# Performance work log

Measured on AMD Instinct MI355X. Metric: run time of the kernel, lower is better.

Reference implementation:

```python
import jax, jax.numpy as jnp
import numpy as np

B, T, C, H = 4, 2048, 1024, 16
D = C // H  # head_dim = 64


def setup_inputs() -> dict:
    key = jax.random.key(0)
    ks = jax.random.split(key, 5)
    s = 0.02
    return {
        "x": jax.random.normal(ks[0], (B, T, C), dtype=jnp.float32),
        "w_qkv": jax.random.normal(ks[1], (C, 3 * C), dtype=jnp.float32) * s,
        "b_qkv": jnp.zeros((3 * C,), dtype=jnp.float32),
        "w_proj": jax.random.normal(ks[2], (C, C), dtype=jnp.float32) * s,
        "b_proj": jnp.zeros((C,), dtype=jnp.float32),
    }


def reference(x, w_qkv, b_qkv, w_proj, b_proj):
    Bx, Tx, Cx = x.shape
    qkv = x @ w_qkv + b_qkv                      # [B,T,3C]
    q, k, v = jnp.split(qkv, 3, axis=-1)
    # [B,T,C] -> [B,H,T,D]
    q = q.reshape(Bx, Tx, H, D).transpose(0, 2, 1, 3)
    k = k.reshape(Bx, Tx, H, D).transpose(0, 2, 1, 3)
    v = v.reshape(Bx, Tx, H, D).transpose(0, 2, 1, 3)
    scale = 1.0 / np.sqrt(D).astype(np.float32)
    attn = jnp.einsum('bhqd,bhkd->bhqk', q, k) * scale   # [B,H,T,T]
    causal = jnp.tril(jnp.ones((Tx, Tx), dtype=bool))
    attn = jnp.where(causal[None, None], attn, -jnp.inf)
    attn = jax.nn.softmax(attn, axis=-1)
    out = jnp.einsum('bhqk,bhkd->bhqd', attn, v)          # [B,H,T,D]
    out = out.transpose(0, 2, 1, 3).reshape(Bx, Tx, Cx)   # [B,T,C]
    return out @ w_proj + b_proj
```

## Files before the change

kernel.cpp:

```cpp
#include <hip/hip_runtime.h>
#include <hip/hip_bf16.h>
#include <math.h>

using bf16 = __hip_bfloat16;
typedef __bf16 bf16x8 __attribute__((ext_vector_type(8)));
typedef float  f32x4  __attribute__((ext_vector_type(4)));
typedef unsigned short ushort8 __attribute__((ext_vector_type(8)));
typedef unsigned uint4v __attribute__((ext_vector_type(4)));

#define DEV __device__ __forceinline__

DEV void gld_lds16(const void* g, void* l) {
    __builtin_amdgcn_global_load_lds((const __attribute__((address_space(1))) void*)g,
                                     (__attribute__((address_space(3))) void*)l,
                                     16, 0, 0);
}

__global__ __launch_bounds__(256) void prep(const float* __restrict__ x,
                                            bf16* __restrict__ xb,
                                            const float* __restrict__ w_qkv,
                                            bf16* __restrict__ wqkvT,
                                            const float* __restrict__ w_proj,
                                            bf16* __restrict__ wprojT) {
    __shared__ float tile[32][33];
    int blk = blockIdx.x;
    int tid = threadIdx.x;
    if (blk < 8192) {
        int i = blk * 256 + tid;
        float4 f = ((const float4*)x)[i];
        __align__(8) bf16 o[4] = {__float2bfloat16(f.x), __float2bfloat16(f.y),
                                  __float2bfloat16(f.z), __float2bfloat16(f.w)};
        ((uint64_t*)xb)[i] = *(const uint64_t*)o;
        return;
    }
    const float* in;
    bf16* out;
    int R, Cn, bx, by;
    if (blk < 11264) {
        int bid = blk - 8192;
        in = w_qkv; out = wqkvT; R = 1024; Cn = 3072;
        bx = (bid % 96) * 32; by = (bid / 96) * 32;
    } else {
        int bid = blk - 11264;
        in = w_proj; out = wprojT; R = 1024; Cn = 1024;
        bx = (bid % 32) * 32; by = (bid / 32) * 32;
    }
    int tx = tid & 31, ty = tid >> 5;
    for (int i = ty; i < 32; i += 8)
        tile[i][tx] = in[(size_t)(by + i) * Cn + bx + tx];
    __syncthreads();
    for (int i = ty; i < 32; i += 8)
        out[(size_t)(bx + i) * R + by + tx] = __float2bfloat16(tile[tx][i]);
}

__global__ __launch_bounds__(256) void gemm_qkv(const bf16* __restrict__ A,
                                                const bf16* __restrict__ Bt,
                                                const float* __restrict__ bias,
                                                bf16* __restrict__ qb,
                                                bf16* __restrict__ kb,
                                                bf16* __restrict__ vTb) {
    constexpr int K = 1024, T = 2048;
    constexpr float CS = 0.18033688f;
    __shared__ __align__(16) bf16 SM[4][128 * 32];
    bf16* Et = &SM[0][0];
    int tid = threadIdx.x;
    int lane = tid & 63, w = tid >> 6;
    int wm = w >> 1, wn = w & 1;
    int l15 = lane & 15, quad = lane >> 4;
    int m0 = blockIdx.x * 128, n0 = blockIdx.y * 128;
    int l3 = l15 & 3;

    int e0 = tid * 8, e1 = (256 + tid) * 8;
    int r0 = e0 >> 5, c0 = ((((e0 >> 3) & 3) ^ (r0 & 3)) << 3);
    int r1 = e1 >> 5, c1 = ((((e1 >> 3) & 3) ^ (r1 & 3)) << 3);

    f32x4 acc[4][4] = {};

    auto STAGE = [&](int buf, int kc) {
        gld_lds16(A  + (size_t)(m0 + r0) * K + kc + c0, &SM[buf][e0]);
        gld_lds16(A  + (size_t)(m0 + r1) * K + kc + c1, &SM[buf][e1]);
        gld_lds16(Bt + (size_t)(n0 + r0) * K + kc + c0, &SM[2 + buf][e0]);
        gld_lds16(Bt + (size_t)(n0 + r1) * K + kc + c1, &SM[2 + buf][e1]);
    };
    auto COMP = [&](int buf) {
        bf16x8 af[4], bfr[4];
        for (int i = 0; i < 4; ++i)
            af[i] = *(const bf16x8*)&SM[buf][(wm * 64 + i * 16 + l15) * 32 + ((quad ^ l3) << 3)];
        for (int j = 0; j < 4; ++j)
            bfr[j] = *(const bf16x8*)&SM[2 + buf][(wn * 64 + j * 16 + l15) * 32 + ((quad ^ l3) << 3)];
        for (int i = 0; i < 4; ++i)
            for (int j = 0; j < 4; ++j)
                acc[i][j] = __builtin_amdgcn_mfma_f32_16x16x32_bf16(af[i], bfr[j], acc[i][j], 0, 0, 0);
    };

    STAGE(0, 0);
    for (int t = 0; t < K / 64; ++t) {
        int k0 = t * 64;
        __syncthreads();
        STAGE(1, k0 + 32);
        COMP(0);
        __syncthreads();
        if (t + 1 < K / 64) STAGE(0, k0 + 64);
        COMP(1);
    }

    int mode = (blockIdx.y < 8) ? 0 : (blockIdx.y < 16 ? 1 : 2);
    float bv[4];
    for (int j = 0; j < 4; ++j)
        bv[j] = bias[n0 + wn * 64 + j * 16 + l15];
    float scl = (mode == 0) ? CS : 1.0f;

    for (int i = 0; i < 4; ++i) {
        __syncthreads();
        for (int j = 0; j < 4; ++j)
            for (int v = 0; v < 4; ++v)
                Et[(wm * 16 + quad * 4 + v) * 136 + wn * 64 + j * 16 + l15] =
                    __float2bfloat16((acc[i][j][v] + bv[j]) * scl);
        __syncthreads();
        if (mode < 2) {
            int r = tid >> 3, cc = (tid & 7) * 16;
            int m = m0 + i * 16 + (r < 16 ? r : r + 48);
            int b = m >> 11, t = m & 2047;
            int n = (n0 & 1023) + cc;
            int h = n >> 6, d = n & 63;
            bf16* dst = (mode == 0 ? qb : kb) + (((size_t)(b * 16 + h)) * T + t) * 64 + d;
            ushort8 u0 = *(const ushort8*)&Et[r * 136 + cc];
            ushort8 u1 = *(const ushort8*)&Et[r * 136 + cc + 8];
            *(ushort8*)dst = u0;
            *(ushort8*)(dst + 8) = u1;
        } else {
            int run = tid >> 7, d = tid & 127;
            int t0 = m0 + i * 16 + run * 64;
            int b = t0 >> 11, tt = t0 & 2047;
            int n = (n0 & 1023) + d;
            int h = n >> 6, dd = n & 63;
            __align__(16) bf16 tmp[16];
            for (int jj = 0; jj < 16; ++jj)
                tmp[jj] = Et[(run * 16 + jj) * 136 + d];
            bf16* dst = vTb + (((size_t)(b * 16 + h)) * 64 + dd) * T + tt;
            *(ushort8*)dst = *(const ushort8*)tmp;
            *(ushort8*)(dst + 8) = *(const ushort8*)(tmp + 8);
        }
    }
}

__global__ __launch_bounds__(256, 4) void flash_attn(const bf16* __restrict__ qb,
                                                     const bf16* __restrict__ kbuf,
                                                     const bf16* __restrict__ vT,
                                                     bf16* __restrict__ ob) {
    constexpr int T = 2048;
    __shared__ __align__(16) bf16 Kl[2][64 * 64];
    __shared__ __align__(16) bf16 Vl[64 * 64];
    int tid = threadIdx.x;
    int lane = tid & 63, w = tid >> 6;
    int l15 = lane & 15, quad = lane >> 4;

    int g = blockIdx.x;
    int quarter = g >> 8;
    int j = (g >> 6) & 3;
    int bh = g & 63;
    int xq;
    switch (quarter) {
        case 0:  xq = 15 - j; break;
        case 1:  xq = 8 + j;  break;
        case 2:  xq = 4 + j;  break;
        default: xq = 3 - j;  break;
    }
    int q0 = xq << 7;
    const bf16* qbase = qb   + (size_t)bh * T * 64;
    const bf16* kbase = kbuf + (size_t)bh * T * 64;
    const bf16* vbase = vT   + (size_t)bh * 64 * T;

    int qg[2];
    bf16x8 qa[2][2];
#pragma unroll
    for (int s = 0; s < 2; ++s) {
        qg[s] = q0 + w * 32 + s * 16 + l15;
#pragma unroll
        for (int c = 0; c < 2; ++c)
            qa[s][c] = *(const bf16x8*)(qbase + (size_t)qg[s] * 64 + c * 32 + quad * 8);
    }

    bf16x8 ones;
#pragma unroll
    for (int i = 0; i < 8; ++i) ones[i] = (__bf16)1.0f;

    f32x4 O[2][4] = {};
    f32x4 O1[2] = {};
    int h7 = l15 & 7;

    int off0 = tid * 8, off1 = (256 + tid) * 8;
    int r0 = off0 >> 6, cb0 = (off0 >> 3) & 7;
    int r1 = off1 >> 6, cb1 = (off1 >> 3) & 7;
    int kc0 = (cb0 ^ (r0 & 7)) << 3, kc1 = (cb1 ^ (r1 & 7)) << 3;

    int nit = 2 * xq + 2;

    bf16x8 vr0 = *(const bf16x8*)(vbase + (size_t)r0 * T + kc0);
    bf16x8 vr1 = *(const bf16x8*)(vbase + (size_t)r1 * T + kc1);
    gld_lds16(kbase + (size_t)r0 * 64 + kc0, &Kl[0][off0]);
    gld_lds16(kbase + (size_t)r1 * 64 + kc1, &Kl[0][off1]);
    *(bf16x8*)&Vl[off0] = vr0;
    *(bf16x8*)&Vl[off1] = vr1;

    for (int t = 0; t < nit; ++t) {
        int cur = t & 1;
        __syncthreads();
        bool pre = (t + 1 < nit);
        if (pre) {
            int kb2 = (t + 1) << 6, nxt = cur ^ 1;
            vr0 = *(const bf16x8*)(vbase + (size_t)r0 * T + kb2 + kc0);
            vr1 = *(const bf16x8*)(vbase + (size_t)r1 * T + kb2 + kc1);
            gld_lds16(kbase + (size_t)(kb2 + r0) * 64 + kc0, &Kl[nxt][off0]);
            gld_lds16(kbase + (size_t)(kb2 + r1) * 64 + kc1, &Kl[nxt][off1]);
        }
        int kb = t << 6;
        bool maskt = (t >= nit - 2);

        unsigned Dq[2][4][2];
#pragma unroll
        for (int jn = 0; jn < 4; ++jn) {
            int row = jn * 16 + l15;
            bf16x8 a0 = *(const bf16x8*)&Kl[cur][row * 64 + ((quad ^ h7) << 3)];
            bf16x8 a1 = *(const bf16x8*)&Kl[cur][row * 64 + (((4 + quad) ^ h7) << 3)];
            f32x4 sa[2] = {};
            __builtin_amdgcn_s_setprio(1);
            sa[0] = __builtin_amdgcn_mfma_f32_16x16x32_bf16(a0, qa[0][0], sa[0], 0, 0, 0);
            sa[0] = __builtin_amdgcn_mfma_f32_16x16x32_bf16(a1, qa[0][1], sa[0], 0, 0, 0);
            sa[1] = __builtin_amdgcn_mfma_f32_16x16x32_bf16(a0, qa[1][0], sa[1], 0, 0, 0);
            sa[1] = __builtin_amdgcn_mfma_f32_16x16x32_bf16(a1, qa[1][1], sa[1], 0, 0, 0);
            __builtin_amdgcn_s_setprio(0);
#pragma unroll
            for (int s = 0; s < 2; ++s) {
                float p[4];
#pragma unroll
                for (int v = 0; v < 4; ++v) {
                    float e = __builtin_amdgcn_exp2f(sa[s][v]);
                    if (maskt) {
                        int key = kb + jn * 16 + quad * 4 + v;
                        e = (key <= qg[s]) ? e : 0.f;
                    }
                    p[v] = e;
                }
                unsigned lo, hi;
                asm("v_cvt_pk_bf16_f32 %0, %1, %2" : "=v"(lo) : "v"(p[0]), "v"(p[1]));
                asm("v_cvt_pk_bf16_f32 %0, %1, %2" : "=v"(hi) : "v"(p[2]), "v"(p[3]));
                Dq[s][jn][0] = lo;
                Dq[s][jn][1] = hi;
            }
        }

        bf16x8 pf[2][2];
#pragma unroll
        for (int s = 0; s < 2; ++s)
#pragma unroll
            for (int c = 0; c < 2; ++c) {
                uint4v wv;
#pragma unroll
                for (int h = 0; h < 2; ++h) {
                    unsigned X = Dq[s][2 * c][h];
                    unsigned Y = Dq[s][2 * c + 1][h];
                    asm("v_permlane32_swap_b32 %0, %1" : "+v"(X), "+v"(Y));
                    asm("v_permlane16_swap_b32 %0, %1" : "+v"(X), "+v"(Y));
                    wv[h]     = X;
                    wv[2 + h] = Y;
                }
                pf[s][c] = __builtin_bit_cast(bf16x8, wv);
            }

        __builtin_amdgcn_s_setprio(1);
#pragma unroll
        for (int s = 0; s < 2; ++s) {
            O1[s] = __builtin_amdgcn_mfma_f32_16x16x32_bf16(pf[s][0], ones, O1[s], 0, 0, 0);
            O1[s] = __builtin_amdgcn_mfma_f32_16x16x32_bf16(pf[s][1], ones, O1[s], 0, 0, 0);
        }
        __builtin_amdgcn_s_setprio(0);

#pragma unroll
        for (int jd = 0; jd < 4; ++jd) {
            int vrow = jd * 16 + l15;
            bf16x8 v0 = *(const bf16x8*)&Vl[vrow * 64 + ((quad ^ h7) << 3)];
            bf16x8 v1 = *(const bf16x8*)&Vl[vrow * 64 + (((4 + quad) ^ h7) << 3)];
            __builtin_amdgcn_s_setprio(1);
            O[0][jd] = __builtin_amdgcn_mfma_f32_16x16x32_bf16(pf[0][0], v0, O[0][jd], 0, 0, 0);
            O[0][jd] = __builtin_amdgcn_mfma_f32_16x16x32_bf16(pf[0][1], v1, O[0][jd], 0, 0, 0);
            O[1][jd] = __builtin_amdgcn_mfma_f32_16x16x32_bf16(pf[1][0], v0, O[1][jd], 0, 0, 0);
            O[1][jd] = __builtin_amdgcn_mfma_f32_16x16x32_bf16(pf[1][1], v1, O[1][jd], 0, 0, 0);
            __builtin_amdgcn_s_setprio(0);
        }

        __builtin_amdgcn_s_barrier();
        if (pre) {
            *(bf16x8*)&Vl[off0] = vr0;
            *(bf16x8*)&Vl[off1] = vr1;
        }
    }

    int b = bh >> 4, h = bh & 15;
#pragma unroll
    for (int s = 0; s < 2; ++s) {
        float linv[4];
#pragma unroll
        for (int v = 0; v < 4; ++v) linv[v] = 1.f / O1[s][v];
#pragma unroll
        for (int jd = 0; jd < 4; ++jd) {
#pragma unroll
            for (int v = 0; v < 4; ++v) {
                int qr = q0 + w * 32 + s * 16 + quad * 4 + v;
                ob[((size_t)(b * T + qr)) * 1024 + h * 64 + jd * 16 + l15] =
                    __float2bfloat16(O[s][jd][v] * linv[v]);
            }
        }
    }
}

__global__ __launch_bounds__(256) void gemm_proj(const bf16* __restrict__ A,
                                                 const bf16* __restrict__ Bt,
                                                 const float* __restrict__ bias,
                                                 float* __restrict__ out) {
    constexpr int K = 1024, N = 1024;
    __shared__ __align__(16) bf16 SM[4][128 * 32];
    int tid = threadIdx.x;
    int lane = tid & 63, w = tid >> 6;
    int wm = w >> 1, wn = w & 1;
    int l15 = lane & 15, quad = lane >> 4;
    int m0 = blockIdx.x * 128, n0 = blockIdx.y * 128;
    int l3 = l15 & 3;

    int e0 = tid * 8, e1 = (256 + tid) * 8;
    int r0 = e0 >> 5, c0 = ((((e0 >> 3) & 3) ^ (r0 & 3)) << 3);
    int r1 = e1 >> 5, c1 = ((((e1 >> 3) & 3) ^ (r1 & 3)) << 3);

    f32x4 acc[4][4] = {};

    auto STAGE = [&](int buf, int kc) {
        gld_lds16(A  + (size_t)(m0 + r0) * K + kc + c0, &SM[buf][e0]);
        gld_lds16(A  + (size_t)(m0 + r1) * K + kc + c1, &SM[buf][e1]);
        gld_lds16(Bt + (size_t)(n0 + r0) * K + kc + c0, &SM[2 + buf][e0]);
        gld_lds16(Bt + (size_t)(n0 + r1) * K + kc + c1, &SM[2 + buf][e1]);
    };
    auto COMP = [&](int buf) {
        bf16x8 af[4], bfr[4];
        for (int i = 0; i < 4; ++i)
            af[i] = *(const bf16x8*)&SM[buf][(wm * 64 + i * 16 + l15) * 32 + ((quad ^ l3) << 3)];
        for (int j = 0; j < 4; ++j)
            bfr[j] = *(const bf16x8*)&SM[2 + buf][(wn * 64 + j * 16 + l15) * 32 + ((quad ^ l3) << 3)];
        for (int i = 0; i < 4; ++i)
            for (int j = 0; j < 4; ++j)
                acc[i][j] = __builtin_amdgcn_mfma_f32_16x16x32_bf16(af[i], bfr[j], acc[i][j], 0, 0, 0);
    };

    STAGE(0, 0);
    for (int t = 0; t < K / 64; ++t) {
        int k0 = t * 64;
        __syncthreads();
        STAGE(1, k0 + 32);
        COMP(0);
        __syncthreads();
        if (t + 1 < K / 64) STAGE(0, k0 + 64);
        COMP(1);
    }

    for (int i = 0; i < 4; ++i) {
        int mbase = m0 + wm * 64 + i * 16 + quad * 4;
        for (int j = 0; j < 4; ++j) {
            int n = n0 + wn * 64 + j * 16 + l15;
            float bv = bias[n];
            for (int v = 0; v < 4; ++v)
                out[(size_t)(mbase + v) * N + n] = acc[i][j][v] + bv;
        }
    }
}

extern "C" void kernel_launch(void* const* d_in, const int* in_sizes, int n_in,
                              void* d_out, int out_size, void* d_ws, size_t ws_size,
                              hipStream_t stream) {
    (void)in_sizes; (void)n_in; (void)out_size; (void)ws_size;
    const float* x      = (const float*)d_in[0];
    const float* w_qkv  = (const float*)d_in[1];
    const float* b_qkv  = (const float*)d_in[2];
    const float* w_proj = (const float*)d_in[3];
    const float* b_proj = (const float*)d_in[4];
    float* out = (float*)d_out;

    char* ws = (char*)d_ws;
    bf16* xb     = (bf16*)(ws);
    bf16* wqkvT  = (bf16*)(ws + (16u << 20));
    bf16* wprojT = (bf16*)(ws + (22u << 20));
    bf16* qbuf   = (bf16*)(ws + (24u << 20));
    bf16* kbuf   = (bf16*)(ws + (40u << 20));
    bf16* vTb    = (bf16*)(ws + (72u << 20));
    bf16* ob     = (bf16*)(ws + (56u << 20));

    prep<<<12288, 256, 0, stream>>>(x, xb, w_qkv, wqkvT, w_proj, wprojT);
    gemm_qkv<<<dim3(64, 24), 256, 0, stream>>>(xb, wqkvT, b_qkv, qbuf, kbuf, vTb);
    flash_attn<<<1024, 256, 0, stream>>>(qbuf, kbuf, vTb, ob);
    gemm_proj<<<dim3(64, 8), 256, 0, stream>>>(ob, wprojT, b_proj, out);
}
```

Before: 237.5 us.

## Retile QKV GEMM to 128x256 with 512 threads, 64-wide K stages, swizzled grid

The QKV projection GEMM moves from 128x128 tiles with 256 threads and 32-wide K slices to 128x256 tiles with 512 threads (8 waves), 64-wide K slices, an XOR-swizzled LDS layout over 8 column groups, and a remapped block order that groups blocks along the N dimension for L2 reuse. MFMA sections get raised priority via s_setprio. The aim is to cut global/LDS traffic per flop and halve the number of K-loop barriers. In exchange it uses 96KB of LDS per block, which lowers occupancy, and the epilogue is rewritten for the wider tile. The attention and projection kernels are only moved in the file, not changed.

Result: no change. 240.7 us (+1.4%).

```diff
diff --git a/kernel.cpp b/kernel.cpp
--- a/kernel.cpp
+++ b/kernel.cpp
@@ -53,16 +53,292 @@
         out[(size_t)(bx + i) * R + by + tx] = __float2bfloat16(tile[tx][i]);
 }
 
-__global__ __launch_bounds__(256) void gemm_qkv(const bf16* __restrict__ A,
+__global__ __launch_bounds__(512) void gemm_qkv(const bf16* __restrict__ A,
                                                 const bf16* __restrict__ Bt,
                                                 const float* __restrict__ bias,
                                                 bf16* __restrict__ qb,
                                                 bf16* __restrict__ kb,
                                                 bf16* __restrict__ vTb) {
-    constexpr int K = 1024, T = 2048;
+    constexpr int K = 1024;
     constexpr float CS = 0.18033688f;
+    __shared__ __align__(16) bf16 SM[49152];
+    int tid = threadIdx.x;
+    int lane = tid & 63, wid = tid >> 6;
+    int wm = wid >> 2, wn = wid & 3;
+    int l15 = lane & 15, quad = lane >> 4;
+    int h7 = l15 & 7;
+
+    int wg = blockIdx.x;
+    int swz = (wg & 7) * 96 + (wg >> 3);
+    int bx = swz & 63, by = swz >> 6;
+    int m0 = bx * 128, n0 = by * 256;
+
+    int r0s = tid >> 3;
+    int sc0 = (((tid & 7) ^ (r0s & 7)) << 3);
+
+    f32x4 acc[4][4] = {};
+
+#define STAGE(buf, kt) do {                                                        \
+    gld_lds16(A  + (size_t)(m0 + r0s)       * K + (kt) * 64 + sc0,                 \
+              &SM[(buf) * 8192 + tid * 8]);                                        \
+    gld_lds16(A  + (size_t)(m0 + 64 + r0s)  * K + (kt) * 64 + sc0,                 \
+              &SM[(buf) * 8192 + 4096 + tid * 8]);                                 \
+    gld_lds16(Bt + (size_t)(n0 + r0s)       * K + (kt) * 64 + sc0,                 \
+              &SM[16384 + (buf) * 16384 + tid * 8]);                               \
+    gld_lds16(Bt + (size_t)(n0 + 64 + r0s)  * K + (kt) * 64 + sc0,                 \
+              &SM[16384 + (buf) * 16384 + 4096 + tid * 8]);                        \
+    gld_lds16(Bt + (size_t)(n0 + 128 + r0s) * K + (kt) * 64 + sc0,                 \
+              &SM[16384 + (buf) * 16384 + 8192 + tid * 8]);                        \
+    gld_lds16(Bt + (size_t)(n0 + 192 + r0s) * K + (kt) * 64 + sc0,                 \
+              &SM[16384 + (buf) * 16384 + 12288 + tid * 8]);                       \
+} while (0)
+
+#define COMP(buf) do {                                                             \
+    bf16x8 afr[4][2], bfr[4][2];                                                   \
+    for (int i = 0; i < 4; ++i)                                                    \
+        for (int kc = 0; kc < 2; ++kc)                                             \
+            afr[i][kc] = *(const bf16x8*)&SM[(buf) * 8192 +                        \
+                (wm * 64 + i * 16 + l15) * 64 + (((kc * 4 + quad) ^ h7) << 3)];    \
+    for (int nj = 0; nj < 4; ++nj)                                                 \
+        for (int kc = 0; kc < 2; ++kc)                                             \
+            bfr[nj][kc] = *(const bf16x8*)&SM[16384 + (buf) * 16384 +              \
+                (wn * 64 + nj * 16 + l15) * 64 + (((kc * 4 + quad) ^ h7) << 3)];   \
+    __builtin_amdgcn_s_setprio(1);                                                 \
+    for (int i = 0; i < 4; ++i)                                                    \
+        for (int nj = 0; nj < 4; ++nj)                                             \
+            for (int kc = 0; kc < 2; ++kc)                                         \
+                acc[i][nj] = __builtin_amdgcn_mfma_f32_16x16x32_bf16(              \
+                    afr[i][kc], bfr[nj][kc], acc[i][nj], 0, 0, 0);                 \
+    __builtin_amdgcn_s_setprio(0);                                                 \
+} while (0)
+
+    STAGE(0, 0);
+    for (int t2 = 0; t2 < 8; ++t2) {
+        __syncthreads();
+        STAGE(1, 2 * t2 + 1);
+        COMP(0);
+        __syncthreads();
+        if (t2 < 7) STAGE(0, 2 * t2 + 2);
+        COMP(1);
+    }
+#undef STAGE
+#undef COMP
+
+    int mode = by >> 2;
+    float scl = (mode == 0) ? CS : 1.0f;
+    float bv[4];
+    for (int nj = 0; nj < 4; ++nj)
+        bv[nj] = bias[n0 + wn * 64 + nj * 16 + l15];
+    bf16* Et = &SM[0];
+
+    for (int i = 0; i < 4; ++i) {
+        __syncthreads();
+        for (int nj = 0; nj < 4; ++nj)
+            for (int v = 0; v < 4; ++v)
+                Et[(wm * 16 + quad * 4 + v) * 264 + wn * 64 + nj * 16 + l15] =
+                    __float2bfloat16((acc[i][nj][v] + bv[nj]) * scl);
+        __syncthreads();
+        if (mode < 2) {
+            int r = tid >> 4, ck = tid & 15;
+            int m = m0 + i * 16 + (r < 16 ? r : r + 48);
+            int b = m >> 11, t = m & 2047;
+            int n = (n0 & 1023) + ck * 16;
+            int h = n >> 6, d = n & 63;
+            bf16* dst = (mode == 0 ? qb : kb) + (((size_t)(b * 16 + h)) * 2048 + t) * 64 + d;
+            *(ushort8*)dst       = *(const ushort8*)&Et[r * 264 + ck * 16];
+            *(ushort8*)(dst + 8) = *(const ushort8*)&Et[r * 264 + ck * 16 + 8];
+        } else {
+            int tg = tid >> 8, d = tid & 255;
+            int t0 = m0 + tg * 64 + i * 16;
+            int b = t0 >> 11, tt = t0 & 2047;
+            int n = (n0 & 1023) + d;
+            int h = n >> 6, dd = n & 63;
+            __align__(16) bf16 tmp[16];
+            for (int jj = 0; jj < 16; ++jj)
+                tmp[jj] = Et[(tg * 16 + jj) * 264 + d];
+            bf16* dst = vTb + (((size_t)(b * 16 + h)) * 64 + dd) * 2048 + tt;
+            *(ushort8*)dst       = *(const ushort8*)tmp;
+            *(ushort8*)(dst + 8) = *(const ushort8*)(tmp + 8);
+        }
+    }
+}
+
+__global__ __launch_bounds__(256, 4) void flash_attn(const bf16* __restrict__ qb,
+                                                     const bf16* __restrict__ kbuf,
+                                                     const bf16* __restrict__ vT,
+                                                     bf16* __restrict__ ob) {
+    constexpr int T = 2048;
+    __shared__ __align__(16) bf16 Kl[2][64 * 64];
+    __shared__ __align__(16) bf16 Vl[64 * 64];
+    int tid = threadIdx.x;
+    int lane = tid & 63, w = tid >> 6;
+    int l15 = lane & 15, quad = lane >> 4;
+
+    int g = blockIdx.x;
+    int quarter = g >> 8;
+    int j = (g >> 6) & 3;
+    int bh = g & 63;
+    int xq;
+    switch (quarter) {
+        case 0:  xq = 15 - j; break;
+        case 1:  xq = 8 + j;  break;
+        case 2:  xq = 4 + j;  break;
+        default: xq = 3 - j;  break;
+    }
+    int q0 = xq << 7;
+    const bf16* qbase = qb   + (size_t)bh * T * 64;
+    const bf16* kbase = kbuf + (size_t)bh * T * 64;
+    const bf16* vbase = vT   + (size_t)bh * 64 * T;
+
+    int qg[2];
+    bf16x8 qa[2][2];
+#pragma unroll
+    for (int s = 0; s < 2; ++s) {
+        qg[s] = q0 + w * 32 + s * 16 + l15;
+#pragma unroll
+        for (int c = 0; c < 2; ++c)
+            qa[s][c] = *(const bf16x8*)(qbase + (size_t)qg[s] * 64 + c * 32 + quad * 8);
+    }
+
+    bf16x8 ones;
+#pragma unroll
+    for (int i = 0; i < 8; ++i) ones[i] = (__bf16)1.0f;
+
+    f32x4 O[2][4] = {};
+    f32x4 O1[2] = {};
+    int h7 = l15 & 7;
+
+    int off0 = tid * 8, off1 = (256 + tid) * 8;
+    int r0 = off0 >> 6, cb0 = (off0 >> 3) & 7;
+    int r1 = off1 >> 6, cb1 = (off1 >> 3) & 7;
+    int kc0 = (cb0 ^ (r0 & 7)) << 3, kc1 = (cb1 ^ (r1 & 7)) << 3;
+
+    int nit = 2 * xq + 2;
+
+    bf16x8 vr0 = *(const bf16x8*)(vbase + (size_t)r0 * T + kc0);
+    bf16x8 vr1 = *(const bf16x8*)(vbase + (size_t)r1 * T + kc1);
+    gld_lds16(kbase + (size_t)r0 * 64 + kc0, &Kl[0][off0]);
+    gld_lds16(kbase + (size_t)r1 * 64 + kc1, &Kl[0][off1]);
+    *(bf16x8*)&Vl[off0] = vr0;
+    *(bf16x8*)&Vl[off1] = vr1;
+
+    for (int t = 0; t < nit; ++t) {
+        int cur = t & 1;
+        __syncthreads();
+        bool pre = (t + 1 < nit);
+        if (pre) {
+            int kb2 = (t + 1) << 6, nxt = cur ^ 1;
+            vr0 = *(const bf16x8*)(vbase + (size_t)r0 * T + kb2 + kc0);
+            vr1 = *(const bf16x8*)(vbase + (size_t)r1 * T + kb2 + kc1);
+            gld_lds16(kbase + (size_t)(kb2 + r0) * 64 + kc0, &Kl[nxt][off0]);
+            gld_lds16(kbase + (size_t)(kb2 + r1) * 64 + kc1, &Kl[nxt][off1]);
+        }
+        int kb = t << 6;
+        bool maskt = (t >= nit - 2);
+
+        unsigned Dq[2][4][2];
+#pragma unroll
+        for (int jn = 0; jn < 4; ++jn) {
+            int row = jn * 16 + l15;
+            bf16x8 a0 = *(const bf16x8*)&Kl[cur][row * 64 + ((quad ^ h7) << 3)];
+            bf16x8 a1 = *(const bf16x8*)&Kl[cur][row * 64 + (((4 + quad) ^ h7) << 3)];
+            f32x4 sa[2] = {};
+            __builtin_amdgcn_s_setprio(1);
+            sa[0] = __builtin_amdgcn_mfma_f32_16x16x32_bf16(a0, qa[0][0], sa[0], 0, 0, 0);
+            sa[0] = __builtin_amdgcn_mfma_f32_16x16x32_bf16(a1, qa[0][1], sa[0], 0, 0, 0);
+            sa[1] = __builtin_amdgcn_mfma_f32_16x16x32_bf16(a0, qa[1][0], sa[1], 0, 0, 0);
+            sa[1] = __builtin_amdgcn_mfma_f32_16x16x32_bf16(a1, qa[1][1], sa[1], 0, 0, 0);
+            __builtin_amdgcn_s_setprio(0);
+#pragma unroll
+            for (int s = 0; s < 2; ++s) {
+                float p[4];
+#pragma unroll
+                for (int v = 0; v < 4; ++v) {
+                    float e = __builtin_amdgcn_exp2f(sa[s][v]);
+                    if (maskt) {
+                        int key = kb + jn * 16 + quad * 4 + v;
+                        e = (key <= qg[s]) ? e : 0.f;
+                    }
+                    p[v] = e;
+                }
+                unsigned lo, hi;
+                asm("v_cvt_pk_bf16_f32 %0, %1, %2" : "=v"(lo) : "v"(p[0]), "v"(p[1]));
+                asm("v_cvt_pk_bf16_f32 %0, %1, %2" : "=v"(hi) : "v"(p[2]), "v"(p[3]));
+                Dq[s][jn][0] = lo;
+                Dq[s][jn][1] = hi;
+            }
+        }
+
+        bf16x8 pf[2][2];
+#pragma unroll
+        for (int s = 0; s < 2; ++s)
+#pragma unroll
+            for (int c = 0; c < 2; ++c) {
+                uint4v wv;
+#pragma unroll
+                for (int h = 0; h < 2; ++h) {
+                    unsigned X = Dq[s][2 * c][h];
+                    unsigned Y = Dq[s][2 * c + 1][h];
+                    asm("v_permlane32_swap_b32 %0, %1" : "+v"(X), "+v"(Y));
+                    asm("v_permlane16_swap_b32 %0, %1" : "+v"(X), "+v"(Y));
+                    wv[h]     = X;
+                    wv[2 + h] = Y;
+                }
+                pf[s][c] = __builtin_bit_cast(bf16x8, wv);
+            }
+
+        __builtin_amdgcn_s_setprio(1);
+#pragma unroll
+        for (int s = 0; s < 2; ++s) {
+            O1[s] = __builtin_amdgcn_mfma_f32_16x16x32_bf16(pf[s][0], ones, O1[s], 0, 0, 0);
+            O1[s] = __builtin_amdgcn_mfma_f32_16x16x32_bf16(pf[s][1], ones, O1[s], 0, 0, 0);
+        }
+        __builtin_amdgcn_s_setprio(0);
+
+#pragma unroll
+        for (int jd = 0; jd < 4; ++jd) {
+            int vrow = jd * 16 + l15;
+            bf16x8 v0 = *(const bf16x8*)&Vl[vrow * 64 + ((quad ^ h7) << 3)];
+            bf16x8 v1 = *(const bf16x8*)&Vl[vrow * 64 + (((4 + quad) ^ h7) << 3)];
+            __builtin_amdgcn_s_setprio(1);
+            O[0][jd] = __builtin_amdgcn_mfma_f32_16x16x32_bf16(pf[0][0], v0, O[0][jd], 0, 0, 0);
+            O[0][jd] = __builtin_amdgcn_mfma_f32_16x16x32_bf16(pf[0][1], v1, O[0][jd], 0, 0, 0);
+            O[1][jd] = __builtin_amdgcn_mfma_f32_16x16x32_bf16(pf[1][0], v0, O[1][jd], 0, 0, 0);
+            O[1][jd] = __builtin_amdgcn_mfma_f32_16x16x32_bf16(pf[1][1], v1, O[1][jd], 0, 0, 0);
+            __builtin_amdgcn_s_setprio(0);
+        }
+
+        __builtin_amdgcn_s_barrier();
+        if (pre) {
+            *(bf16x8*)&Vl[off0] = vr0;
+            *(bf16x8*)&Vl[off1] = vr1;
+        }
+    }
+
+    int b = bh >> 4, h = bh & 15;
+#pragma unroll
+    for (int s = 0; s < 2; ++s) {
+        float linv[4];
+#pragma unroll
+        for (int v = 0; v < 4; ++v) linv[v] = 1.f / O1[s][v];
+#pragma unroll
+        for (int jd = 0; jd < 4; ++jd) {
+#pragma unroll
+            for (int v = 0; v < 4; ++v) {
+                int qr = q0 + w * 32 + s * 16 + quad * 4 + v;
+                ob[((size_t)(b * T + qr)) * 1024 + h * 64 + jd * 16 + l15] =
+                    __float2bfloat16(O[s][jd][v] * linv[v]);
+            }
+        }
+    }
+}
+
+__global__ __launch_bounds__(256) void gemm_proj(const bf16* __restrict__ A,
+                                                 const bf16* __restrict__ Bt,
+                                                 const float* __restrict__ bias,
+                                                 float* __restrict__ out) {
+    constexpr int K = 1024, N = 1024;
     __shared__ __align__(16) bf16 SM[4][128 * 32];
-    bf16* Et = &SM[0][0];
     int tid = threadIdx.x;
     int lane = tid & 63, w = tid >> 6;
     int wm = w >> 1, wn = w & 1;
@@ -104,263 +380,6 @@
         COMP(1);
     }
 
-    int mode = (blockIdx.y < 8) ? 0 : (blockIdx.y < 16 ? 1 : 2);
-    float bv[4];
-    for (int j = 0; j < 4; ++j)
-        bv[j] = bias[n0 + wn * 64 + j * 16 + l15];
-    float scl = (mode == 0) ? CS : 1.0f;
-
-    for (int i = 0; i < 4; ++i) {
-        __syncthreads();
-        for (int j = 0; j < 4; ++j)
-            for (int v = 0; v < 4; ++v)
-                Et[(wm * 16 + quad * 4 + v) * 136 + wn * 64 + j * 16 + l15] =
-                    __float2bfloat16((acc[i][j][v] + bv[j]) * scl);
-        __syncthreads();
-        if (mode < 2) {
-            int r = tid >> 3, cc = (tid & 7) * 16;
-            int m = m0 + i * 16 + (r < 16 ? r : r + 48);
-            int b = m >> 11, t = m & 2047;
-            int n = (n0 & 1023) + cc;
-            int h = n >> 6, d = n & 63;
-            bf16* dst = (mode == 0 ? qb : kb) + (((size_t)(b * 16 + h)) * T + t) * 64 + d;
-            ushort8 u0 = *(const ushort8*)&Et[r * 136 + cc];
-            ushort8 u1 = *(const ushort8*)&Et[r * 136 + cc + 8];
-            *(ushort8*)dst = u0;
-            *(ushort8*)(dst + 8) = u1;
-        } else {
-            int run = tid >> 7, d = tid & 127;
-            int t0 = m0 + i * 16 + run * 64;
-            int b = t0 >> 11, tt = t0 & 2047;
-            int n = (n0 & 1023) + d;
-            int h = n >> 6, dd = n & 63;
-            __align__(16) bf16 tmp[16];
-            for (int jj = 0; jj < 16; ++jj)
-                tmp[jj] = Et[(run * 16 + jj) * 136 + d];
-            bf16* dst = vTb + (((size_t)(b * 16 + h)) * 64 + dd) * T + tt;
-            *(ushort8*)dst = *(const ushort8*)tmp;
-            *(ushort8*)(dst + 8) = *(const ushort8*)(tmp + 8);
-        }
-    }
-}
-
-__global__ __launch_bounds__(256, 4) void flash_attn(const bf16* __restrict__ qb,
-                                                     const bf16* __restrict__ kbuf,
-                                                     const bf16* __restrict__ vT,
-                                                     bf16* __restrict__ ob) {
-    constexpr int T = 2048;
-    __shared__ __align__(16) bf16 Kl[2][64 * 64];
-    __shared__ __align__(16) bf16 Vl[64 * 64];
-    int tid = threadIdx.x;
-    int lane = tid & 63, w = tid >> 6;
-    int l15 = lane & 15, quad = lane >> 4;
-
-    int g = blockIdx.x;
-    int quarter = g >> 8;
-    int j = (g >> 6) & 3;
-    int bh = g & 63;
-    int xq;
-    switch (quarter) {
-        case 0:  xq = 15 - j; break;
-        case 1:  xq = 8 + j;  break;
-        case 2:  xq = 4 + j;  break;
-        default: xq = 3 - j;  break;
-    }
-    int q0 = xq << 7;
-    const bf16* qbase = qb   + (size_t)bh * T * 64;
-    const bf16* kbase = kbuf + (size_t)bh * T * 64;
-    const bf16* vbase = vT   + (size_t)bh * 64 * T;
-
-    int qg[2];
-    bf16x8 qa[2][2];
-#pragma unroll
-    for (int s = 0; s < 2; ++s) {
-        qg[s] = q0 + w * 32 + s * 16 + l15;
-#pragma unroll
-        for (int c = 0; c < 2; ++c)
-            qa[s][c] = *(const bf16x8*)(qbase + (size_t)qg[s] * 64 + c * 32 + quad * 8);
-    }
-
-    bf16x8 ones;
-#pragma unroll
-    for (int i = 0; i < 8; ++i) ones[i] = (__bf16)1.0f;
-
-    f32x4 O[2][4] = {};
-    f32x4 O1[2] = {};
-    int h7 = l15 & 7;
-
-    int off0 = tid * 8, off1 = (256 + tid) * 8;
-    int r0 = off0 >> 6, cb0 = (off0 >> 3) & 7;
-    int r1 = off1 >> 6, cb1 = (off1 >> 3) & 7;
-    int kc0 = (cb0 ^ (r0 & 7)) << 3, kc1 = (cb1 ^ (r1 & 7)) << 3;
-
-    int nit = 2 * xq + 2;
-
-    bf16x8 vr0 = *(const bf16x8*)(vbase + (size_t)r0 * T + kc0);
-    bf16x8 vr1 = *(const bf16x8*)(vbase + (size_t)r1 * T + kc1);
-    gld_lds16(kbase + (size_t)r0 * 64 + kc0, &Kl[0][off0]);
-    gld_lds16(kbase + (size_t)r1 * 64 + kc1, &Kl[0][off1]);
-    *(bf16x8*)&Vl[off0] = vr0;
-    *(bf16x8*)&Vl[off1] = vr1;
-
-    for (int t = 0; t < nit; ++t) {
-        int cur = t & 1;
-        __syncthreads();
-        bool pre = (t + 1 < nit);
-        if (pre) {
-            int kb2 = (t + 1) << 6, nxt = cur ^ 1;
-            vr0 = *(const bf16x8*)(vbase + (size_t)r0 * T + kb2 + kc0);
-            vr1 = *(const bf16x8*)(vbase + (size_t)r1 * T + kb2 + kc1);
-            gld_lds16(kbase + (size_t)(kb2 + r0) * 64 + kc0, &Kl[nxt][off0]);
-            gld_lds16(kbase + (size_t)(kb2 + r1) * 64 + kc1, &Kl[nxt][off1]);
-        }
-        int kb = t << 6;
-        bool maskt = (t >= nit - 2);
-
-        unsigned Dq[2][4][2];
-#pragma unroll
-        for (int jn = 0; jn < 4; ++jn) {
-            int row = jn * 16 + l15;
-            bf16x8 a0 = *(const bf16x8*)&Kl[cur][row * 64 + ((quad ^ h7) << 3)];
-            bf16x8 a1 = *(const bf16x8*)&Kl[cur][row * 64 + (((4 + quad) ^ h7) << 3)];
-            f32x4 sa[2] = {};
-            __builtin_amdgcn_s_setprio(1);
-            sa[0] = __builtin_amdgcn_mfma_f32_16x16x32_bf16(a0, qa[0][0], sa[0], 0, 0, 0);
-            sa[0] = __builtin_amdgcn_mfma_f32_16x16x32_bf16(a1, qa[0][1], sa[0], 0, 0, 0);
-            sa[1] = __builtin_amdgcn_mfma_f32_16x16x32_bf16(a0, qa[1][0], sa[1], 0, 0, 0);
-            sa[1] = __builtin_amdgcn_mfma_f32_16x16x32_bf16(a1, qa[1][1], sa[1], 0, 0, 0);
-            __builtin_amdgcn_s_setprio(0);
-#pragma unroll
-            for (int s = 0; s < 2; ++s) {
-                float p[4];
-#pragma unroll
-                for (int v = 0; v < 4; ++v) {
-                    float e = __builtin_amdgcn_exp2f(sa[s][v]);
-                    if (maskt) {
-                        int key = kb + jn * 16 + quad * 4 + v;
-                        e = (key <= qg[s]) ? e : 0.f;
-                    }
-                    p[v] = e;
-                }
-                unsigned lo, hi;
-                asm("v_cvt_pk_bf16_f32 %0, %1, %2" : "=v"(lo) : "v"(p[0]), "v"(p[1]));
-                asm("v_cvt_pk_bf16_f32 %0, %1, %2" : "=v"(hi) : "v"(p[2]), "v"(p[3]));
-                Dq[s][jn][0] = lo;
-                Dq[s][jn][1] = hi;
-            }
-        }
-
-        bf16x8 pf[2][2];
-#pragma unroll
-        for (int s = 0; s < 2; ++s)
-#pragma unroll
-            for (int c = 0; c < 2; ++c) {
-                uint4v wv;
-#pragma unroll
-                for (int h = 0; h < 2; ++h) {
-                    unsigned X = Dq[s][2 * c][h];
-                    unsigned Y = Dq[s][2 * c + 1][h];
-                    asm("v_permlane32_swap_b32 %0, %1" : "+v"(X), "+v"(Y));
-                    asm("v_permlane16_swap_b32 %0, %1" : "+v"(X), "+v"(Y));
-                    wv[h]     = X;
-                    wv[2 + h] = Y;
-                }
-                pf[s][c] = __builtin_bit_cast(bf16x8, wv);
-            }
-
-        __builtin_amdgcn_s_setprio(1);
-#pragma unroll
-        for (int s = 0; s < 2; ++s) {
-            O1[s] = __builtin_amdgcn_mfma_f32_16x16x32_bf16(pf[s][0], ones, O1[s], 0, 0, 0);
-            O1[s] = __builtin_amdgcn_mfma_f32_16x16x32_bf16(pf[s][1], ones, O1[s], 0, 0, 0);
-        }
-        __builtin_amdgcn_s_setprio(0);
-
-#pragma unroll
-        for (int jd = 0; jd < 4; ++jd) {
-            int vrow = jd * 16 + l15;
-            bf16x8 v0 = *(const bf16x8*)&Vl[vrow * 64 + ((quad ^ h7) << 3)];
-            bf16x8 v1 = *(const bf16x8*)&Vl[vrow * 64 + (((4 + quad) ^ h7) << 3)];
-            __builtin_amdgcn_s_setprio(1);
-            O[0][jd] = __builtin_amdgcn_mfma_f32_16x16x32_bf16(pf[0][0], v0, O[0][jd], 0, 0, 0);
-            O[0][jd] = __builtin_amdgcn_mfma_f32_16x16x32_bf16(pf[0][1], v1, O[0][jd], 0, 0, 0);
-            O[1][jd] = __builtin_amdgcn_mfma_f32_16x16x32_bf16(pf[1][0], v0, O[1][jd], 0, 0, 0);
-            O[1][jd] = __builtin_amdgcn_mfma_f32_16x16x32_bf16(pf[1][1], v1, O[1][jd], 0, 0, 0);
-            __builtin_amdgcn_s_setprio(0);
-        }
-
-        __builtin_amdgcn_s_barrier();
-        if (pre) {
-            *(bf16x8*)&Vl[off0] = vr0;
-            *(bf16x8*)&Vl[off1] = vr1;
-        }
-    }
-
-    int b = bh >> 4, h = bh & 15;
-#pragma unroll
-    for (int s = 0; s < 2; ++s) {
-        float linv[4];
-#pragma unroll
-        for (int v = 0; v < 4; ++v) linv[v] = 1.f / O1[s][v];
-#pragma unroll
-        for (int jd = 0; jd < 4; ++jd) {
-#pragma unroll
-            for (int v = 0; v < 4; ++v) {
-                int qr = q0 + w * 32 + s * 16 + quad * 4 + v;
-                ob[((size_t)(b * T + qr)) * 1024 + h * 64 + jd * 16 + l15] =
-                    __float2bfloat16(O[s][jd][v] * linv[v]);
-            }
-        }
-    }
-}
-
-__global__ __launch_bounds__(256) void gemm_proj(const bf16* __restrict__ A,
-                                                 const bf16* __restrict__ Bt,
-                                                 const float* __restrict__ bias,
-                                                 float* __restrict__ out) {
-    constexpr int K = 1024, N = 1024;
-    __shared__ __align__(16) bf16 SM[4][128 * 32];
-    int tid = threadIdx.x;
-    int lane = tid & 63, w = tid >> 6;
-    int wm = w >> 1, wn = w & 1;
-    int l15 = lane & 15, quad = lane >> 4;
-    int m0 = blockIdx.x * 128, n0 = blockIdx.y * 128;
-    int l3 = l15 & 3;
-
-    int e0 = tid * 8, e1 = (256 + tid) * 8;
-    int r0 = e0 >> 5, c0 = ((((e0 >> 3) & 3) ^ (r0 & 3)) << 3);
-    int r1 = e1 >> 5, c1 = ((((e1 >> 3) & 3) ^ (r1 & 3)) << 3);
-
-    f32x4 acc[4][4] = {};
-
-    auto STAGE = [&](int buf, int kc) {
-        gld_lds16(A  + (size_t)(m0 + r0) * K + kc + c0, &SM[buf][e0]);
-        gld_lds16(A  + (size_t)(m0 + r1) * K + kc + c1, &SM[buf][e1]);
-        gld_lds16(Bt + (size_t)(n0 + r0) * K + kc + c0, &SM[2 + buf][e0]);
-        gld_lds16(Bt + (size_t)(n0 + r1) * K + kc + c1, &SM[2 + buf][e1]);
-    };
-    auto COMP = [&](int buf) {
-        bf16x8 af[4], bfr[4];
-        for (int i = 0; i < 4; ++i)
-            af[i] = *(const bf16x8*)&SM[buf][(wm * 64 + i * 16 + l15) * 32 + ((quad ^ l3) << 3)];
-        for (int j = 0; j < 4; ++j)
-            bfr[j] = *(const bf16x8*)&SM[2 + buf][(wn * 64 + j * 16 + l15) * 32 + ((quad ^ l3) << 3)];
-        for (int i = 0; i < 4; ++i)
-            for (int j = 0; j < 4; ++j)
-                acc[i][j] = __builtin_amdgcn_mfma_f32_16x16x32_bf16(af[i], bfr[j], acc[i][j], 0, 0, 0);
-    };
-
-    STAGE(0, 0);
-    for (int t = 0; t < K / 64; ++t) {
-        int k0 = t * 64;
-        __syncthreads();
-        STAGE(1, k0 + 32);
-        COMP(0);
-        __syncthreads();
-        if (t + 1 < K / 64) STAGE(0, k0 + 64);
-        COMP(1);
-    }
-
     for (int i = 0; i < 4; ++i) {
         int mbase = m0 + wm * 64 + i * 16 + quad * 4;
         for (int j = 0; j < 4; ++j) {
@@ -393,7 +412,7 @@
     bf16* ob     = (bf16*)(ws + (56u << 20));
 
     prep<<<12288, 256, 0, stream>>>(x, xb, w_qkv, wqkvT, w_proj, wprojT);
-    gemm_qkv<<<dim3(64, 24), 256, 0, stream>>>(xb, wqkvT, b_qkv, qbuf, kbuf, vTb);
+    gemm_qkv<<<768, 512, 0, stream>>>(xb, wqkvT, b_qkv, qbuf, kbuf, vTb);
     flash_attn<<<1024, 256, 0, stream>>>(qbuf, kbuf, vTb, ob);
     gemm_proj<<<dim3(64, 8), 256, 0, stream>>>(ob, wprojT, b_proj, out);
 }
```
